# Optimization experiments

Measured on AMD Instinct MI355X. Metric: run time of the kernel, lower is better.

The kernel has to match this reference:

```python
import jax, jax.numpy as jnp
import numpy as np

K_NN = 32
LN_EPS = 1e-5
P_JOINT = 0.95      # safety_priorities['structural_joints']
P_PLATFORM = 0.9    # safety_priorities['working_platforms']


def _sqdist(a, b):
    # a:[B,M,3], b:[B,N,3] -> [B,M,N] squared euclidean distances
    return jnp.maximum(jnp.sum(a * a, -1)[:, :, None] + jnp.sum(b * b, -1)[:, None, :]
                       - 2.0 * jnp.einsum('bmd,bnd->bmn', a, b), 0.0)


def _gather(arr, idx):
    # arr:[B,N,D], idx:[B,C] -> [B,C,D]
    B, C = idx.shape
    return jnp.take_along_axis(arr, jnp.broadcast_to(idx[:, :, None], (B, C, arr.shape[-1])), axis=1)


def _fps(coords, num_samples):
    # iterative farthest point sampling (deterministic start at index 0)
    B, N, _ = coords.shape
    start = jnp.zeros((B,), jnp.int32)
    dist0 = jnp.full((B, N), jnp.inf, coords.dtype)
    samp0 = jnp.zeros((B, num_samples), jnp.int32)

    def body(i, carry):
        dist, samp, last = carry
        last_pts = _gather(coords, last[:, None])                 # [B,1,3]
        d = jnp.sqrt(jnp.sum((coords - last_pts) ** 2, -1))       # [B,N]
        dist = jnp.minimum(dist, d)
        nxt = jnp.argmax(dist, 1).astype(jnp.int32)
        dist = dist.at[jnp.arange(B), nxt].set(0.0)
        samp = samp.at[:, i].set(nxt)
        return dist, samp, nxt

    _, samp, _ = jax.lax.fori_loop(1, num_samples, body, (dist0, samp0, start))
    return samp


def _safety(coords, scale):
    # per-point safety score [B,N], computed on the full point cloud (as in original)
    N = coords.shape[1]
    z = coords[:, :, 2]
    if scale == 'global':
        return 1.0 + jax.nn.sigmoid((z - z.mean(1, keepdims=True)) / 5.0) * P_JOINT
    if scale == 'component':
        zv = jnp.var(z, axis=1, keepdims=True, ddof=1)            # torch.var is unbiased
        return jnp.broadcast_to(1.0 + jnp.exp(-zv / 0.1) * P_PLATFORM, z.shape)
    # detail: full NxN cdist -> connection density (dist < 0.5  <=>  sqdist < 0.25)
    d2 = _sqdist(coords, coords)                                  # [B,N,N]
    density = jnp.sum(d2 < 0.25, -1).astype(coords.dtype)
    return 1.0 + density / N * P_JOINT


def _select_scale(features, coords, C, S, W1, b1, W2, b2, scale):
    idx = _fps(coords, C)                     # [B,C]
    cfeat = _gather(features, idx)            # [B,C,D]
    ccoord = _gather(coords, idx)             # [B,C,3]
    # kNN max-pooled local features (computed by original module; not used downstream)
    knn_d2 = _sqdist(ccoord, coords)          # [B,C,N]
    _, knn = jax.lax.top_k(-knn_d2, K_NN)
    _local = jax.vmap(lambda f, i: f[i])(features, knn).max(2)    # [B,C,D]
    # per-center safety score: per-point score gathered at FPS centers
    safety = jnp.take_along_axis(_safety(coords, scale), idx, axis=1)  # [B,C]
    # selector MLP: Linear -> ReLU -> Linear -> Sigmoid
    probs = jax.nn.sigmoid(jnp.maximum(cfeat @ W1.T + b1, 0.0) @ W2.T + b2)  # [B,C,S]
    final = probs.mean(-1) * safety           # [B,C] per-center score
    _, top = jax.lax.top_k(final, S)          # [B,S]
    return _gather(cfeat, top)                # [B,S,D]


def _forward(pf, pc, g_W1, g_b1, g_W2, g_b2, c_W1, c_b1, c_W2, c_b2,
             d_W1, d_b1, d_W2, d_b2, p_W1, p_b1, p_W2, p_b2, ln_g, ln_b):
    g = _select_scale(pf, pc, 256, 16, g_W1, g_b1, g_W2, g_b2, 'global')
    c = _select_scale(pf, pc, 128, 16, c_W1, c_b1, c_W2, c_b2, 'component')
    d = _select_scale(pf, pc, 64, 8, d_W1, d_b1, d_W2, d_b2, 'detail')
    toks = jnp.concatenate([g, c, d], 1)      # [B,40,D]
    # prompt_mlp: Linear(D,D/2) -> ReLU -> Linear(D/2,D) -> LayerNorm(D)
    h = jnp.maximum(toks @ p_W1.T + p_b1, 0.0) @ p_W2.T + p_b2
    mu = h.mean(-1, keepdims=True)
    var = h.var(-1, keepdims=True)
    return (h - mu) * jax.lax.rsqrt(var + LN_EPS) * ln_g + ln_b


def setup_inputs() -> dict:
    key = jax.random.key(0)
    B, N, D = 2, 8192, 768
    ks = iter(jax.random.split(key, 32))

    def nrm(shape, s=0.02):
        return jax.random.normal(next(ks), shape, jnp.float32) * s

    inp = {
        'point_features': jax.random.normal(next(ks), (B, N, D), jnp.float32),
        'point_coords': jax.random.normal(next(ks), (B, N, 3), jnp.float32) * 2.0,
    }
    for p, C, S in [('g', 256, 16), ('c', 128, 16), ('d', 64, 8)]:
        inp[p + '_W1'] = nrm((C, D)); inp[p + '_b1'] = jnp.zeros((C,), jnp.float32)
        inp[p + '_W2'] = nrm((S, C)); inp[p + '_b2'] = jnp.zeros((S,), jnp.float32)
    inp['p_W1'] = nrm((D // 2, D)); inp['p_b1'] = jnp.zeros((D // 2,), jnp.float32)
    inp['p_W2'] = nrm((D, D // 2)); inp['p_b2'] = jnp.zeros((D,), jnp.float32)
    inp['ln_g'] = jnp.ones((D,), jnp.float32); inp['ln_b'] = jnp.zeros((D,), jnp.float32)
    return inp


def reference(point_features, point_coords, g_W1, g_b1, g_W2, g_b2,
              c_W1, c_b1, c_W2, c_b2, d_W1, d_b1, d_W2, d_b2,
              p_W1, p_b1, p_W2, p_b2, ln_g, ln_b):
    return _forward(point_features, point_coords, g_W1, g_b1, g_W2, g_b2,
                    c_W1, c_b1, c_W2, c_b2, d_W1, d_b1, d_W2, d_b2,
                    p_W1, p_b1, p_W2, p_b2, ln_g, ln_b)
```

## Files before the change

kernel.cpp:

```cpp
#include <hip/hip_runtime.h>
#include <math.h>

#define N_PTS 8192
#define D_FEAT 768

typedef float v2f __attribute__((ext_vector_type(2)));

__device__ __forceinline__ float wred_max_f32(float x) {
    int v = __float_as_int(x), o;
    o = __builtin_amdgcn_update_dpp(0, v, 0x111, 0xf, 0xf, false); v = __float_as_int(fmaxf(__int_as_float(v), __int_as_float(o)));
    o = __builtin_amdgcn_update_dpp(0, v, 0x112, 0xf, 0xf, false); v = __float_as_int(fmaxf(__int_as_float(v), __int_as_float(o)));
    o = __builtin_amdgcn_update_dpp(0, v, 0x114, 0xf, 0xf, false); v = __float_as_int(fmaxf(__int_as_float(v), __int_as_float(o)));
    o = __builtin_amdgcn_update_dpp(0, v, 0x118, 0xf, 0xf, false); v = __float_as_int(fmaxf(__int_as_float(v), __int_as_float(o)));
    o = __builtin_amdgcn_update_dpp(0, v, 0x142, 0xa, 0xf, false); v = __float_as_int(fmaxf(__int_as_float(v), __int_as_float(o)));
    o = __builtin_amdgcn_update_dpp(0, v, 0x143, 0xc, 0xf, false); v = __float_as_int(fmaxf(__int_as_float(v), __int_as_float(o)));
    return __int_as_float(__builtin_amdgcn_readlane(v, 63));
}
__device__ __forceinline__ int wred_min_i32(int x) {
    int v = x, o;
    o = __builtin_amdgcn_update_dpp(0x7fffffff, v, 0x111, 0xf, 0xf, false); v = (o < v) ? o : v;
    o = __builtin_amdgcn_update_dpp(0x7fffffff, v, 0x112, 0xf, 0xf, false); v = (o < v) ? o : v;
    o = __builtin_amdgcn_update_dpp(0x7fffffff, v, 0x114, 0xf, 0xf, false); v = (o < v) ? o : v;
    o = __builtin_amdgcn_update_dpp(0x7fffffff, v, 0x118, 0xf, 0xf, false); v = (o < v) ? o : v;
    o = __builtin_amdgcn_update_dpp(0x7fffffff, v, 0x142, 0xa, 0xf, false); v = (o < v) ? o : v;
    o = __builtin_amdgcn_update_dpp(0x7fffffff, v, 0x143, 0xc, 0xf, false); v = (o < v) ? o : v;
    return __builtin_amdgcn_readlane(v, 63);
}
__device__ __forceinline__ float wred_add_f32(float x) {
    int v = __float_as_int(x), o;
    o = __builtin_amdgcn_update_dpp(0, v, 0x111, 0xf, 0xf, false); v = __float_as_int(__int_as_float(v) + __int_as_float(o));
    o = __builtin_amdgcn_update_dpp(0, v, 0x112, 0xf, 0xf, false); v = __float_as_int(__int_as_float(v) + __int_as_float(o));
    o = __builtin_amdgcn_update_dpp(0, v, 0x114, 0xf, 0xf, false); v = __float_as_int(__int_as_float(v) + __int_as_float(o));
    o = __builtin_amdgcn_update_dpp(0, v, 0x118, 0xf, 0xf, false); v = __float_as_int(__int_as_float(v) + __int_as_float(o));
    o = __builtin_amdgcn_update_dpp(0, v, 0x142, 0xa, 0xf, false); v = __float_as_int(__int_as_float(v) + __int_as_float(o));
    o = __builtin_amdgcn_update_dpp(0, v, 0x143, 0xc, 0xf, false); v = __float_as_int(__int_as_float(v) + __int_as_float(o));
    return __int_as_float(__builtin_amdgcn_readlane(v, 63));
}

#define DPP64_STEP(cur, ctrl, rmask)                                                        \
    {                                                                                       \
        unsigned _h = (unsigned)__builtin_amdgcn_update_dpp(0, (int)(unsigned)((cur) >> 32), ctrl, rmask, 0xf, false); \
        unsigned _l = (unsigned)__builtin_amdgcn_update_dpp(0, (int)(unsigned)(cur), ctrl, rmask, 0xf, false);         \
        unsigned long long _o = ((unsigned long long)_h << 32) | _l;                        \
        cur = (_o > (cur)) ? _o : (cur);                                                    \
    }

__global__ __launch_bounds__(512, 2) __attribute__((amdgpu_waves_per_eu(2)))
void fps_kernel(const float* __restrict__ coords,
                int* __restrict__ idx_all,
                float* __restrict__ safety_all) {
#pragma clang fp contract(off)
    const int b = blockIdx.x;
    const int t = threadIdx.x;
    const float* cb = coords + (size_t)b * N_PTS * 3;

    v2f px2[8], py2[8], pz2[8], m2p[8];
#pragma unroll
    for (int j = 0; j < 8; j++) {
        int p0 = t + (2 * j) * 512, p1 = t + (2 * j + 1) * 512;
        px2[j].x = cb[p0 * 3 + 0]; px2[j].y = cb[p1 * 3 + 0];
        py2[j].x = cb[p0 * 3 + 1]; py2[j].y = cb[p1 * 3 + 1];
        pz2[j].x = cb[p0 * 3 + 2]; pz2[j].y = cb[p1 * 3 + 2];
        m2p[j].x = INFINITY; m2p[j].y = INFINITY;
    }
    __shared__ float cbl4[N_PTS * 4];
    __shared__ unsigned long long skey[2][8];
    __shared__ int sel[256];
    __shared__ float r1s[8], r2s[8];
#pragma unroll
    for (int j = 0; j < 8; j++) {
        int p0 = t + (2 * j) * 512, p1 = t + (2 * j + 1) * 512;
        *(float4*)&cbl4[p0 * 4] = make_float4(px2[j].x, py2[j].x, pz2[j].x, 0.f);
        *(float4*)&cbl4[p1 * 4] = make_float4(px2[j].y, py2[j].y, pz2[j].y, 0.f);
    }
    if (t == 0) sel[0] = 0;
    float lx = cb[0], ly = cb[1], lz = cb[2];
    __syncthreads();

    const int lane = t & 63, w = t >> 6;
    for (int i = 1; i < 256; i++) {
        v2f Lx = {lx, lx}, Ly = {ly, ly}, Lz = {lz, lz};
#pragma unroll
        for (int j = 0; j < 8; j++) {
            v2f dx = px2[j] - Lx, dy = py2[j] - Ly, dz = pz2[j] - Lz;
            v2f d2 = dx * dx + dy * dy + dz * dz;
            m2p[j] = __builtin_elementwise_min(m2p[j], d2);
        }
        v2f q[4];
#pragma unroll
        for (int j = 0; j < 4; j++) q[j] = __builtin_elementwise_max(m2p[j], m2p[j + 4]);
        q[0] = __builtin_elementwise_max(q[0], q[2]);
        q[1] = __builtin_elementwise_max(q[1], q[3]);
        q[0] = __builtin_elementwise_max(q[0], q[1]);
        float c2 = fmaxf(q[0].x, q[0].y);
        int ci[8];
#pragma unroll
        for (int j = 0; j < 8; j++) {
            int a  = (m2p[j].x == c2) ? (2 * j)     : 0x7fff;
            int bb = (m2p[j].y == c2) ? (2 * j + 1) : 0x7fff;
            ci[j] = (a < bb) ? a : bb;
        }
#pragma unroll
        for (int j = 0; j < 4; j++) ci[j] = min(ci[j], ci[j + 4]);
        int bk = min(min(ci[0], ci[1]), min(ci[2], ci[3]));
        float thi = c2 * 0.9999995f;
        int tot = 0;
#pragma unroll
        for (int j = 0; j < 8; j++) {
            tot += __popcll(__ballot(m2p[j].x >= thi));
            tot += __popcll(__ballot(m2p[j].y >= thi));
        }
        float smax;
        if (tot > 64) {
            smax = -1.f; bk = 0;
#pragma unroll
            for (int k = 0; k < 16; k++) {
                float mk = (k & 1) ? m2p[k >> 1].y : m2p[k >> 1].x;
                float s = sqrtf(mk);
                if (s > smax) { smax = s; bk = k; }
            }
        } else {
            smax = sqrtf(c2);
        }
        int bi = t + bk * 512;
        float mred = wred_max_f32(smax);
        unsigned long long ball = __ballot(smax == mred);
        int bi_win;
        if (__popcll(ball) == 1) {
            int ls = (int)__builtin_ctzll(ball);
            bi_win = __builtin_amdgcn_readlane(bi, ls);
        } else {
            int cand = (smax == mred) ? bi : 0x7fffffff;
            bi_win = wred_min_i32(cand);
        }
        unsigned long long key = ((unsigned long long)__float_as_uint(mred) << 32)
                               | (unsigned)(0xFFFFFFFFu - (unsigned)bi_win);
        if (lane == 63) skey[i & 1][w] = key;
        __syncthreads();
        const int par = i & 1;
        unsigned long long k8 = skey[par][lane & 7];
        int cidx = (int)(0xFFFFFFFFu - (unsigned)k8);
        float spec = 0.f;
        if (lane < 24) spec = cbl4[cidx * 4 + (lane >> 3)];
        DPP64_STEP(k8, 0x111, 0xf)
        DPP64_STEP(k8, 0x112, 0xf)
        DPP64_STEP(k8, 0x114, 0xf)
        unsigned klo = (unsigned)__builtin_amdgcn_readlane((int)(unsigned)k8, 7);
        int fbi = (int)(0xFFFFFFFFu - klo);
        int ww = (fbi & 511) >> 6;
        lx = __int_as_float(__builtin_amdgcn_readlane(__float_as_int(spec), ww));
        ly = __int_as_float(__builtin_amdgcn_readlane(__float_as_int(spec), 8 + ww));
        lz = __int_as_float(__builtin_amdgcn_readlane(__float_as_int(spec), 16 + ww));
        if (t == 0) sel[i] = fbi;
    }

    __syncthreads();
    if (t < 256) {
        int v = sel[t];
        idx_all[b * 256 + t] = v;
        if (t < 128) idx_all[512 + b * 128 + t] = v;
        if (t < 64)  idx_all[768 + b * 64 + t] = v;
    }

    float s1 = 0.f, s2 = 0.f;
#pragma unroll
    for (int j = 0; j < 8; j++) {
        s1 += pz2[j].x; s2 += pz2[j].x * pz2[j].x;
        s1 += pz2[j].y; s2 += pz2[j].y * pz2[j].y;
    }
    s1 = wred_add_f32(s1);
    s2 = wred_add_f32(s2);
    if (lane == 0) { r1s[w] = s1; r2s[w] = s2; }
    __syncthreads();
    float S1 = ((r1s[0] + r1s[1]) + (r1s[2] + r1s[3])) + ((r1s[4] + r1s[5]) + (r1s[6] + r1s[7]));
    float S2 = ((r2s[0] + r2s[1]) + (r2s[2] + r2s[3])) + ((r2s[4] + r2s[5]) + (r2s[6] + r2s[7]));
    float mean = S1 / 8192.0f;
    float var1 = (S2 - S1 * S1 / 8192.0f) / 8191.0f;
    float scomp = 1.0f + expf(-var1 / 0.1f) * 0.9f;
    if (t < 256) {
        int p = sel[t];
        float z = cbl4[p * 4 + 2];
        safety_all[b * 256 + t] = 1.0f + (1.0f / (1.0f + expf(-((z - mean) / 5.0f)))) * 0.95f;
        if (t < 128) safety_all[512 + b * 128 + t] = scomp;
    }
}

#define W1_GEMM(RT)                                                            \
  {                                                                            \
    const int jg = t >> 2, rp = t & 3;                                         \
    const float* wb = W1 + (size_t)(jg * RT) * 768 + rp * 192;                 \
    float4 acc[RT][8];                                                         \
    _Pragma("unroll") for (int a = 0; a < RT; a++)                             \
      _Pragma("unroll") for (int r = 0; r < 8; r++)                            \
        acc[a][r] = make_float4(0.f, 0.f, 0.f, 0.f);                           \
    for (int s = 0; s < 192; s += 4) {                                         \
      float4 xv[8];                                                            \
      _Pragma("unroll") for (int r = 0; r < 8; r++)                            \
        xv[r] = *(const float4*)&xt[r * 772 + rp * 192 + s];                   \
      _Pragma("unroll") for (int a = 0; a < RT; a++) {                         \
        float4 wv = *(const float4*)&wb[(size_t)a * 768 + s];                  \
        _Pragma("unroll") for (int r = 0; r < 8; r++) {                        \
          acc[a][r].x = fmaf(wv.x, xv[r].x, acc[a][r].x);                      \
          acc[a][r].y = fmaf(wv.y, xv[r].y, acc[a][r].y);                      \
          acc[a][r].z = fmaf(wv.z, xv[r].z, acc[a][r].z);                      \
          acc[a][r].w = fmaf(wv.w, xv[r].w, acc[a][r].w);                      \
        }                                                                      \
      }                                                                        \
    }                                                                          \
    _Pragma("unroll") for (int a = 0; a < RT; a++)                             \
      _Pragma("unroll") for (int r = 0; r < 8; r++)                            \
        part[rp * 2048 + (jg * RT + a) * 8 + r] =                              \
            (acc[a][r].x + acc[a][r].y) + (acc[a][r].z + acc[a][r].w);         \
  }

__global__ __launch_bounds__(256) void score_kernel(
    const float* __restrict__ feat, const float* __restrict__ coords,
    const float* __restrict__ gW1, const float* __restrict__ gb1,
    const float* __restrict__ gW2, const float* __restrict__ gb2,
    const float* __restrict__ cW1, const float* __restrict__ cb1,
    const float* __restrict__ cW2, const float* __restrict__ cb2,
    const float* __restrict__ dW1, const float* __restrict__ db1,
    const float* __restrict__ dW2, const float* __restrict__ db2,
    const int* __restrict__ idx_all, const float* __restrict__ safety_all,
    float* __restrict__ final_all) {
    int bid = blockIdx.x;
    int b, c0, C, S, off;
    const float *W1, *b1, *W2, *b2;
    if (bid < 64)      { C = 256; S = 16; W1 = gW1; b1 = gb1; W2 = gW2; b2 = gb2; b = bid >> 5; c0 = (bid & 31) * 8; off = 0; }
    else if (bid < 96) { int r = bid - 64; C = 128; S = 16; W1 = cW1; b1 = cb1; W2 = cW2; b2 = cb2; b = r >> 4; c0 = (r & 15) * 8; off = 512; }
    else               { int r = bid - 96; C = 64;  S = 8;  W1 = dW1; b1 = db1; W2 = dW2; b2 = db2; b = r >> 3; c0 = (r & 7) * 8; off = 768; }
    const bool isdet = (bid >= 96);

    __shared__ float xt[8 * 772];
    __shared__ float h1s[8 * 260];
    __shared__ float part[4 * 2048];
    __shared__ float ps[8 * 16];
    __shared__ int pid[8];
    __shared__ float dpart[4][8];
    __shared__ float sdens[8];
    const int t = threadIdx.x;
    if (t < 8) pid[t] = idx_all[off + b * C + c0 + t];
    __syncthreads();

    if (isdet) {
#pragma clang fp contract(off)
        float cx[8], cy[8], cz[8], cc[8];
#pragma unroll
        for (int c = 0; c < 8; c++) {
            const float* cp = coords + ((size_t)b * N_PTS + pid[c]) * 3;
            cx[c] = cp[0]; cy[c] = cp[1]; cz[c] = cp[2];
            cc[c] = cx[c] * cx[c] + cy[c] * cy[c] + cz[c] * cz[c];
        }
        int cnt[8];
#pragma unroll
        for (int c = 0; c < 8; c++) cnt[c] = 0;
        const float* cbl = coords + (size_t)b * N_PTS * 3;
        for (int k = 0; k < 32; k++) {
            int q = t + k * 256;
            float x = cbl[q * 3], y = cbl[q * 3 + 1], z = cbl[q * 3 + 2];
            float pp = x * x + y * y + z * z;
#pragma unroll
            for (int c = 0; c < 8; c++) {
                float dot = cx[c] * x + cy[c] * y + cz[c] * z;
                float d2 = (cc[c] + pp) - 2.0f * dot;
                if (d2 < 0.25f) cnt[c]++;
            }
        }
        int wv = t >> 6;
#pragma unroll
        for (int c = 0; c < 8; c++) {
            float s = wred_add_f32((float)cnt[c]);
            if ((t & 63) == 0) dpart[wv][c] = s;
        }
    }

    for (int r = 0; r < 8; r++) {
        const float* src = feat + ((size_t)b * N_PTS + pid[r]) * D_FEAT;
        for (int c = t; c < 768; c += 256) xt[r * 772 + c] = src[c];
    }
    __syncthreads();
    if (isdet && t < 8) {
        float tot = dpart[0][t] + dpart[1][t] + dpart[2][t] + dpart[3][t];
        sdens[t] = 1.0f + (tot / 8192.0f) * 0.95f;
    }

    if (C == 256)      W1_GEMM(4)
    else if (C == 128) W1_GEMM(2)
    else               W1_GEMM(1)
    __syncthreads();
    for (int u = t; u < C * 8; u += 256) {
        int row = u >> 3;
        float sum = (part[u] + part[2048 + u]) + (part[4096 + u] + part[6144 + u]) + b1[row];
        h1s[(u & 7) * 260 + row] = fmaxf(sum, 0.f);
    }
    __syncthreads();

    if (t < 8 * S) {
        int r = t / S, s = t % S;
        float4 a = make_float4(0, 0, 0, 0);
        for (int k = 0; k < C; k += 4) {
            float4 wv = *(const float4*)&W2[s * C + k];
            float4 h = *(const float4*)&h1s[r * 260 + k];
            a.x = fmaf(wv.x, h.x, a.x); a.y = fmaf(wv.y, h.y, a.y);
            a.z = fmaf(wv.z, h.z, a.z); a.w = fmaf(wv.w, h.w, a.w);
        }
        float logit = (a.x + a.y) + (a.z + a.w) + b2[s];
        ps[r * 16 + s] = 1.0f / (1.0f + expf(-logit));
    }
    __syncthreads();
    if (t < 8) {
        float m = 0.f;
        for (int s = 0; s < S; s++) m += ps[t * 16 + s];
        m /= (float)S;
        float saf = isdet ? sdens[t] : safety_all[off + b * C + c0 + t];
        final_all[off + b * C + c0 + t] = m * saf;
    }
}


__global__ __launch_bounds__(64) void topk_kernel(
    const float* __restrict__ final_all, const int* __restrict__ idx_all,
    int* __restrict__ tok) {
    int bid = blockIdx.x;
    int b = bid / 3, sc = bid % 3;
    int C    = (sc == 0) ? 256 : (sc == 1) ? 128 : 64;
    int off  = (sc == 0) ? 0 : (sc == 1) ? 512 : 768;
    int base = (sc == 0) ? 0 : (sc == 1) ? 16 : 32;
    int S    = (sc == 2) ? 8 : 16;
    int t = threadIdx.x;
    float v[4];
#pragma unroll
    for (int j = 0; j < 4; j++) {
        int ii = t + j * 64;
        v[j] = (ii < C) ? final_all[off + b * C + ii] : -INFINITY;
    }
    for (int s = 0; s < S; s++) {
        float bd = v[0]; int bj = 0;
#pragma unroll
        for (int j = 1; j < 4; j++) if (v[j] > bd) { bd = v[j]; bj = j; }
        int bi2 = t + bj * 64;
        float m = wred_max_f32(bd);
        int cand = (bd == m) ? bi2 : 0x7fffffff;
        int wi = wred_min_i32(cand);
        if (t == (wi & 63)) {
#pragma unroll
            for (int j = 0; j < 4; j++) if (j == (wi >> 6)) v[j] = -INFINITY;
        }
        if (t == 0) tok[b * 40 + base + s] = idx_all[off + b * C + wi];
    }
}

__global__ __launch_bounds__(320) void h_kernel(
    const float* __restrict__ feat, const int* __restrict__ tok,
    const float* __restrict__ pW1, const float* __restrict__ pb1,
    float* __restrict__ h_buf) {
    int bid = blockIdx.x;
    int b = bid / 48, js = bid % 48;
    int t = threadIdx.x;
    int tk = t % 40, jr = t / 40;
    int j = js * 8 + jr;
    int p = tok[b * 40 + tk];
    const float* x = feat + ((size_t)b * N_PTS + p) * D_FEAT;
    const float* wrow = pW1 + (size_t)j * 768;
    float4 a = make_float4(0, 0, 0, 0);
    for (int k = 0; k < 768; k += 4) {
        float4 wv = *(const float4*)&wrow[k];
        float4 xv = *(const float4*)&x[k];
        a.x = fmaf(wv.x, xv.x, a.x); a.y = fmaf(wv.y, xv.y, a.y);
        a.z = fmaf(wv.z, xv.z, a.z); a.w = fmaf(wv.w, xv.w, a.w);
    }
    float v = (a.x + a.y) + (a.z + a.w) + pb1[j];
    h_buf[((size_t)b * 40 + tk) * 384 + j] = fmaxf(v, 0.f);
}

__global__ __launch_bounds__(320) void out_kernel(
    const float* __restrict__ h_buf,
    const float* __restrict__ pW2, const float* __restrict__ pb2,
    float* __restrict__ pre_buf) {
    int bid = blockIdx.x;
    int b = bid / 96, os = bid % 96;
    int t = threadIdx.x;
    int tk = t % 40, orr = t / 40;
    int o = os * 8 + orr;
    const float* h = h_buf + ((size_t)b * 40 + tk) * 384;
    const float* wrow = pW2 + (size_t)o * 384;
    float4 a = make_float4(0, 0, 0, 0);
    for (int k = 0; k < 384; k += 4) {
        float4 wv = *(const float4*)&wrow[k];
        float4 hv = *(const float4*)&h[k];
        a.x = fmaf(wv.x, hv.x, a.x); a.y = fmaf(wv.y, hv.y, a.y);
        a.z = fmaf(wv.z, hv.z, a.z); a.w = fmaf(wv.w, hv.w, a.w);
    }
    pre_buf[((size_t)b * 40 + tk) * 768 + o] = (a.x + a.y) + (a.z + a.w) + pb2[o];
}

__global__ __launch_bounds__(64) void ln_kernel(
    const float* __restrict__ pre_buf,
    const float* __restrict__ lng, const float* __restrict__ lnb,
    float* __restrict__ out) {
    int bid = blockIdx.x;
    int lane = threadIdx.x;
    const float* row = pre_buf + (size_t)bid * 768;
    float v[12], s1 = 0.f, s2 = 0.f;
#pragma unroll
    for (int i = 0; i < 12; i++) {
        v[i] = row[lane + i * 64];
        s1 += v[i]; s2 += v[i] * v[i];
    }
    s1 = wred_add_f32(s1);
    s2 = wred_add_f32(s2);
    float mu = s1 / 768.0f;
    float var = s2 / 768.0f - mu * mu;
    float inv = rsqrtf(var + 1e-5f);
    float* dst = out + (size_t)bid * 768;
#pragma unroll
    for (int i = 0; i < 12; i++) {
        int o = lane + i * 64;
        dst[o] = (v[i] - mu) * inv * lng[o] + lnb[o];
    }
}

extern "C" void kernel_launch(void* const* d_in, const int* in_sizes, int n_in,
                              void* d_out, int out_size, void* d_ws, size_t ws_size,
                              hipStream_t stream) {
    const float* feat   = (const float*)d_in[0];
    const float* coords = (const float*)d_in[1];
    const float* gW1 = (const float*)d_in[2],  *gb1 = (const float*)d_in[3];
    const float* gW2 = (const float*)d_in[4],  *gb2 = (const float*)d_in[5];
    const float* cW1 = (const float*)d_in[6],  *cb1 = (const float*)d_in[7];
    const float* cW2 = (const float*)d_in[8],  *cb2 = (const float*)d_in[9];
    const float* dW1 = (const float*)d_in[10], *db1 = (const float*)d_in[11];
    const float* dW2 = (const float*)d_in[12], *db2 = (const float*)d_in[13];
    const float* pW1 = (const float*)d_in[14], *pb1 = (const float*)d_in[15];
    const float* pW2 = (const float*)d_in[16], *pb2 = (const float*)d_in[17];
    const float* lng = (const float*)d_in[18], *lnb = (const float*)d_in[19];
    float* out = (float*)d_out;

    int*   idx_all    = (int*)d_ws;
    float* safety_all = (float*)d_ws + 896;
    float* final_all  = (float*)d_ws + 1792;
    int*   tok        = (int*)d_ws + 2688;
    float* h_buf      = (float*)d_ws + 2816;
    float* pre_buf    = (float*)d_ws + 33536;

    fps_kernel<<<2, 512, 0, stream>>>(coords, idx_all, safety_all);
    score_kernel<<<112, 256, 0, stream>>>(feat, coords, gW1, gb1, gW2, gb2, cW1, cb1, cW2, cb2,
                                          dW1, db1, dW2, db2, idx_all, safety_all, final_all);
    topk_kernel<<<6, 64, 0, stream>>>(final_all, idx_all, tok);
    h_kernel<<<96, 320, 0, stream>>>(feat, tok, pW1, pb1, h_buf);
    out_kernel<<<192, 320, 0, stream>>>(h_buf, pW2, pb2, pre_buf);
    ln_kernel<<<80, 64, 0, stream>>>(pre_buf, lng, lnb, out);
}
```

Baseline: 525.7 us.

## Fuse topk into h kernel, fuse out-projection with layernorm, pack FPS argmax key

Removes the separate topk kernel by having three waves in each h_kernel block redo the top-k selection into shared memory. It also fuses the second projection with layernorm so each block computes a full 768-wide row and reduces it in-block. In the FPS loop, the value/index argmax is reduced as a single packed 64-bit key via DPP, replacing the max-then-ballot-then-min sequence. This cuts two kernel launches and the intermediate global round trips. In exchange, top-k is recomputed redundantly in 96 blocks, and the out projection drops from 192 blocks to 80.

```diff
diff --git a/kernel.cpp b/kernel.cpp
--- a/kernel.cpp
+++ b/kernel.cpp
@@ -123,18 +123,14 @@
             smax = sqrtf(c2);
         }
         int bi = t + bk * 512;
-        float mred = wred_max_f32(smax);
-        unsigned long long ball = __ballot(smax == mred);
-        int bi_win;
-        if (__popcll(ball) == 1) {
-            int ls = (int)__builtin_ctzll(ball);
-            bi_win = __builtin_amdgcn_readlane(bi, ls);
-        } else {
-            int cand = (smax == mred) ? bi : 0x7fffffff;
-            bi_win = wred_min_i32(cand);
-        }
-        unsigned long long key = ((unsigned long long)__float_as_uint(mred) << 32)
-                               | (unsigned)(0xFFFFFFFFu - (unsigned)bi_win);
+        unsigned long long key = ((unsigned long long)__float_as_uint(smax) << 32)
+                               | (unsigned)(0xFFFFFFFFu - (unsigned)bi);
+        DPP64_STEP(key, 0x111, 0xf)
+        DPP64_STEP(key, 0x112, 0xf)
+        DPP64_STEP(key, 0x114, 0xf)
+        DPP64_STEP(key, 0x118, 0xf)
+        DPP64_STEP(key, 0x142, 0xa)
+        DPP64_STEP(key, 0x143, 0xc)
         if (lane == 63) skey[i & 1][w] = key;
         __syncthreads();
         const int par = i & 1;
@@ -317,49 +313,48 @@
     }
 }
 
-
-__global__ __launch_bounds__(64) void topk_kernel(
-    const float* __restrict__ final_all, const int* __restrict__ idx_all,
-    int* __restrict__ tok) {
-    int bid = blockIdx.x;
-    int b = bid / 3, sc = bid % 3;
-    int C    = (sc == 0) ? 256 : (sc == 1) ? 128 : 64;
-    int off  = (sc == 0) ? 0 : (sc == 1) ? 512 : 768;
-    int base = (sc == 0) ? 0 : (sc == 1) ? 16 : 32;
-    int S    = (sc == 2) ? 8 : 16;
-    int t = threadIdx.x;
-    float v[4];
-#pragma unroll
-    for (int j = 0; j < 4; j++) {
-        int ii = t + j * 64;
-        v[j] = (ii < C) ? final_all[off + b * C + ii] : -INFINITY;
-    }
-    for (int s = 0; s < S; s++) {
-        float bd = v[0]; int bj = 0;
-#pragma unroll
-        for (int j = 1; j < 4; j++) if (v[j] > bd) { bd = v[j]; bj = j; }
-        int bi2 = t + bj * 64;
-        float m = wred_max_f32(bd);
-        int cand = (bd == m) ? bi2 : 0x7fffffff;
-        int wi = wred_min_i32(cand);
-        if (t == (wi & 63)) {
-#pragma unroll
-            for (int j = 0; j < 4; j++) if (j == (wi >> 6)) v[j] = -INFINITY;
-        }
-        if (t == 0) tok[b * 40 + base + s] = idx_all[off + b * C + wi];
-    }
-}
-
-__global__ __launch_bounds__(320) void h_kernel(
-    const float* __restrict__ feat, const int* __restrict__ tok,
+__global__ __launch_bounds__(320) void hk_kernel(
+    const float* __restrict__ feat, const int* __restrict__ idx_all,
+    const float* __restrict__ final_all,
     const float* __restrict__ pW1, const float* __restrict__ pb1,
     float* __restrict__ h_buf) {
     int bid = blockIdx.x;
     int b = bid / 48, js = bid % 48;
     int t = threadIdx.x;
+    __shared__ int tokp[40];
+    int w = t >> 6, lane = t & 63;
+    if (w < 3) {
+        int sc = w;
+        int C    = (sc == 0) ? 256 : (sc == 1) ? 128 : 64;
+        int off  = (sc == 0) ? 0 : (sc == 1) ? 512 : 768;
+        int base = (sc == 0) ? 0 : (sc == 1) ? 16 : 32;
+        int S    = (sc == 2) ? 8 : 16;
+        float v[4];
+#pragma unroll
+        for (int j = 0; j < 4; j++) {
+            int ii = lane + j * 64;
+            v[j] = (ii < C) ? final_all[off + b * C + ii] : -INFINITY;
+        }
+        for (int s = 0; s < S; s++) {
+            float bd = v[0]; int bj = 0;
+#pragma unroll
+            for (int j = 1; j < 4; j++) if (v[j] > bd) { bd = v[j]; bj = j; }
+            int bi2 = lane + bj * 64;
+            float m = wred_max_f32(bd);
+            int cand = (bd == m) ? bi2 : 0x7fffffff;
+            int wi = wred_min_i32(cand);
+            if (lane == (wi & 63)) {
+#pragma unroll
+                for (int j = 0; j < 4; j++) if (j == (wi >> 6)) v[j] = -INFINITY;
+            }
+            if (lane == 0) tokp[base + s] = idx_all[off + b * C + wi];
+        }
+    }
+    __syncthreads();
+
     int tk = t % 40, jr = t / 40;
     int j = js * 8 + jr;
-    int p = tok[b * 40 + tk];
+    int p = tokp[tk];
     const float* x = feat + ((size_t)b * N_PTS + p) * D_FEAT;
     const float* wrow = pW1 + (size_t)j * 768;
     float4 a = make_float4(0, 0, 0, 0);
@@ -373,50 +368,51 @@
     h_buf[((size_t)b * 40 + tk) * 384 + j] = fmaxf(v, 0.f);
 }
 
-__global__ __launch_bounds__(320) void out_kernel(
+__global__ __launch_bounds__(256) void outln_kernel(
     const float* __restrict__ h_buf,
     const float* __restrict__ pW2, const float* __restrict__ pb2,
-    float* __restrict__ pre_buf) {
-    int bid = blockIdx.x;
-    int b = bid / 96, os = bid % 96;
-    int t = threadIdx.x;
-    int tk = t % 40, orr = t / 40;
-    int o = os * 8 + orr;
-    const float* h = h_buf + ((size_t)b * 40 + tk) * 384;
-    const float* wrow = pW2 + (size_t)o * 384;
-    float4 a = make_float4(0, 0, 0, 0);
-    for (int k = 0; k < 384; k += 4) {
-        float4 wv = *(const float4*)&wrow[k];
-        float4 hv = *(const float4*)&h[k];
-        a.x = fmaf(wv.x, hv.x, a.x); a.y = fmaf(wv.y, hv.y, a.y);
-        a.z = fmaf(wv.z, hv.z, a.z); a.w = fmaf(wv.w, hv.w, a.w);
-    }
-    pre_buf[((size_t)b * 40 + tk) * 768 + o] = (a.x + a.y) + (a.z + a.w) + pb2[o];
-}
-
-__global__ __launch_bounds__(64) void ln_kernel(
-    const float* __restrict__ pre_buf,
     const float* __restrict__ lng, const float* __restrict__ lnb,
     float* __restrict__ out) {
     int bid = blockIdx.x;
-    int lane = threadIdx.x;
-    const float* row = pre_buf + (size_t)bid * 768;
-    float v[12], s1 = 0.f, s2 = 0.f;
-#pragma unroll
-    for (int i = 0; i < 12; i++) {
-        v[i] = row[lane + i * 64];
-        s1 += v[i]; s2 += v[i] * v[i];
-    }
+    int t = threadIdx.x;
+    __shared__ float hs[384];
+    __shared__ float red[8];
+    const float* hrow = h_buf + (size_t)bid * 384;
+    for (int u = t; u < 384; u += 256) hs[u] = hrow[u];
+    __syncthreads();
+
+    float vout[3];
+#pragma unroll
+    for (int a = 0; a < 3; a++) {
+        int o = t + a * 256;
+        const float* wrow = pW2 + (size_t)o * 384;
+        float4 acc = make_float4(0, 0, 0, 0);
+        for (int k = 0; k < 384; k += 4) {
+            float4 wv = *(const float4*)&wrow[k];
+            float4 hv = *(const float4*)&hs[k];
+            acc.x = fmaf(wv.x, hv.x, acc.x); acc.y = fmaf(wv.y, hv.y, acc.y);
+            acc.z = fmaf(wv.z, hv.z, acc.z); acc.w = fmaf(wv.w, hv.w, acc.w);
+        }
+        vout[a] = (acc.x + acc.y) + (acc.z + acc.w) + pb2[o];
+    }
+
+    float s1 = (vout[0] + vout[1]) + vout[2];
+    float s2 = (vout[0] * vout[0] + vout[1] * vout[1]) + vout[2] * vout[2];
     s1 = wred_add_f32(s1);
     s2 = wred_add_f32(s2);
-    float mu = s1 / 768.0f;
-    float var = s2 / 768.0f - mu * mu;
+    int lane = t & 63, wid = t >> 6;
+    if (lane == 0) { red[wid * 2] = s1; red[wid * 2 + 1] = s2; }
+    __syncthreads();
+    float S1 = (red[0] + red[2]) + (red[4] + red[6]);
+    float S2 = (red[1] + red[3]) + (red[5] + red[7]);
+    float mu = S1 / 768.0f;
+    float var = S2 / 768.0f - mu * mu;
     float inv = rsqrtf(var + 1e-5f);
     float* dst = out + (size_t)bid * 768;
 #pragma unroll
-    for (int i = 0; i < 12; i++) {
-        int o = lane + i * 64;
-        dst[o] = (v[i] - mu) * inv * lng[o] + lnb[o];
+    for (int a = 0; a < 3; a++) {
+        int o = t + a * 256;
+        dst[o] = (vout[a] - mu) * inv * lng[o] + lnb[o];
     }
 }
 
@@ -439,15 +435,11 @@
     int*   idx_all    = (int*)d_ws;
     float* safety_all = (float*)d_ws + 896;
     float* final_all  = (float*)d_ws + 1792;
-    int*   tok        = (int*)d_ws + 2688;
-    float* h_buf      = (float*)d_ws + 2816;
-    float* pre_buf    = (float*)d_ws + 33536;
+    float* h_buf      = (float*)d_ws + 2688;
 
     fps_kernel<<<2, 512, 0, stream>>>(coords, idx_all, safety_all);
     score_kernel<<<112, 256, 0, stream>>>(feat, coords, gW1, gb1, gW2, gb2, cW1, cb1, cW2, cb2,
                                           dW1, db1, dW2, db2, idx_all, safety_all, final_all);
-    topk_kernel<<<6, 64, 0, stream>>>(final_all, idx_all, tok);
-    h_kernel<<<96, 320, 0, stream>>>(feat, tok, pW1, pb1, h_buf);
-    out_kernel<<<192, 320, 0, stream>>>(h_buf, pW2, pb2, pre_buf);
-    ln_kernel<<<80, 64, 0, stream>>>(pre_buf, lng, lnb, out);
-}
+    hk_kernel<<<96, 320, 0, stream>>>(feat, idx_all, final_all, pW1, pb1, h_buf);
+    outln_kernel<<<80, 256, 0, stream>>>(h_buf, pW2, pb2, lng, lnb, out);
+}
```

Result: slower. 539.0 us (+2.5%).
